# Performance work log

Hardware: AMD Instinct MI355X
Metric: run time of the kernel (lower is better)

The kernel has to match this reference:

```python
import jax, jax.numpy as jnp
import numpy as np

N, E, G = 50000, 800000, 64
F_IN, H = 128, 256


def setup_inputs() -> dict:
    key = jax.random.key(0)
    ks = jax.random.split(key, 16)
    s = 0.05
    return {
        "x": jax.random.normal(ks[0], (N, F_IN), jnp.float32),
        "edge_index": jax.random.randint(ks[1], (2, E), 0, N, jnp.int32),
        "batch": jnp.sort(jax.random.randint(ks[2], (N,), 0, G, jnp.int32)),
        "W1": jax.random.normal(ks[3], (F_IN, H), jnp.float32) * s,
        "b1": jnp.zeros((H,), jnp.float32),
        "W2": jax.random.normal(ks[4], (H, H), jnp.float32) * s,
        "b2": jnp.zeros((H,), jnp.float32),
        "W3": jax.random.normal(ks[5], (H, H), jnp.float32) * s,
        "b3": jnp.zeros((H,), jnp.float32),
        "Wc1": jax.random.normal(ks[6], (2 * H, 512), jnp.float32) * s,
        "bc1": jnp.zeros((512,), jnp.float32),
        "Wc2": jax.random.normal(ks[7], (512, 256), jnp.float32) * s,
        "bc2": jnp.zeros((256,), jnp.float32),
        "Wc3": jax.random.normal(ks[8], (256, 5), jnp.float32) * s,
        "bc3": jnp.zeros((5,), jnp.float32),
    }


def _gcn_conv(x, src, dst, dis, W, b):
    # PyG GCNConv: h = x W; out = D^{-1/2}(A+I)D^{-1/2} h + b
    h = x @ W                                        # [N, H]
    coef = (dis[src] * dis[dst])[:, None]            # [E, 1]
    agg = jax.ops.segment_sum(h[src] * coef, dst, num_segments=x.shape[0])
    return agg + h * (dis * dis)[:, None] + b        # self-loop term


def reference(x, edge_index, batch, W1, b1, W2, b2, W3, b3,
              Wc1, bc1, Wc2, bc2, Wc3, bc3):
    src, dst = edge_index[0], edge_index[1]
    # degree with self loops (in-degree at dst, as PyG)
    deg = jax.ops.segment_sum(jnp.ones_like(dst, jnp.float32), dst,
                              num_segments=x.shape[0]) + 1.0
    dis = jax.lax.rsqrt(deg)                         # D^{-1/2}

    h = jax.nn.relu(_gcn_conv(x, src, dst, dis, W1, b1))  # dropout=identity (eval)
    h = jax.nn.relu(_gcn_conv(h, src, dst, dis, W2, b2))
    h = jax.nn.relu(_gcn_conv(h, src, dst, dis, W3, b3))

    # global mean / max pool per graph
    cnt = jax.ops.segment_sum(jnp.ones_like(batch, jnp.float32), batch,
                              num_segments=G)
    x_mean = jax.ops.segment_sum(h, batch, num_segments=G) / jnp.maximum(cnt, 1.0)[:, None]
    x_max = jax.ops.segment_max(h, batch, num_segments=G)
    x_max = jnp.where(cnt[:, None] > 0, x_max, 0.0)  # guard empty segments
    g = jnp.concatenate([x_mean, x_max], axis=1)     # [G, 512]

    g = jax.nn.relu(g @ Wc1 + bc1)
    g = jax.nn.relu(g @ Wc2 + bc2)
    return g @ Wc3 + bc3                             # [G, 5]
```

## Files before the change

### kernel.cpp

```cpp
#include <hip/hip_runtime.h>
#include <cstdint>

#define CDIV(a, b) (((a) + (b) - 1) / (b))

typedef short bf16x8 __attribute__((ext_vector_type(8)));
typedef float f32x4 __attribute__((ext_vector_type(4)));

__device__ inline ushort f2bf_rn(float f) {
    uint32_t u = __float_as_uint(f);
    uint32_t rounding = 0x7FFF + ((u >> 16) & 1);
    return (ushort)((u + rounding) >> 16);
}
__device__ inline float bf2f(ushort h) { return __uint_as_float((uint32_t)h << 16); }

__global__ void k_init(int* __restrict__ degc, int N, float* __restrict__ sumbuf,
                       int* __restrict__ maxbuf, int PB) {
    int i = blockIdx.x * blockDim.x + threadIdx.x;
    if (i < N) degc[i] = 0;
    if (i < PB) { sumbuf[i] = 0.f; maxbuf[i] = 0; }
}

__global__ void k_deg(const int* __restrict__ dst, int E, int* __restrict__ degc) {
    int e = blockIdx.x * blockDim.x + threadIdx.x;
    if (e < E) atomicAdd(&degc[dst[e]], 1);
}

__global__ void k_xsplit(const float* __restrict__ x, int n, ushort* __restrict__ xhi) {
    int i = blockIdx.x * blockDim.x + threadIdx.x;
    if (i < n) xhi[i] = f2bf_rn(x[i]);
}

__global__ void k_scan_partial(const int* __restrict__ degc, int N, int* __restrict__ csum) {
    __shared__ int sm[256];
    int t = threadIdx.x;
    int idx = blockIdx.x * 1024 + t * 4;
    int s = 0;
#pragma unroll
    for (int j = 0; j < 4; ++j)
        if (idx + j < N) s += degc[idx + j];
    sm[t] = s;
    __syncthreads();
    for (int off = 128; off > 0; off >>= 1) {
        if (t < off) sm[t] += sm[t + off];
        __syncthreads();
    }
    if (t == 0) csum[blockIdx.x] = sm[0];
}

__global__ void k_scan_chunks(const int* __restrict__ csum, int nch, int* __restrict__ coff,
                              int* __restrict__ row_ptr, int N, int E) {
    if (threadIdx.x == 0 && blockIdx.x == 0) {
        int run = 0;
        for (int i = 0; i < nch; ++i) { coff[i] = run; run += csum[i]; }
        row_ptr[N] = E;
    }
}

__global__ void k_scan_final(const int* __restrict__ degc, int N, const int* __restrict__ coff,
                             int* __restrict__ row_ptr, int* __restrict__ fill,
                             float* __restrict__ dis) {
    __shared__ int sm[256];
    int t = threadIdx.x;
    int idx = blockIdx.x * 1024 + t * 4;
    int v[4];
    int s = 0;
#pragma unroll
    for (int j = 0; j < 4; ++j) {
        v[j] = (idx + j < N) ? degc[idx + j] : 0;
        s += v[j];
    }
    sm[t] = s;
    __syncthreads();
    for (int off = 1; off < 256; off <<= 1) {
        int x = (t >= off) ? sm[t - off] : 0;
        __syncthreads();
        sm[t] += x;
        __syncthreads();
    }
    int excl = sm[t] - s + coff[blockIdx.x];
#pragma unroll
    for (int j = 0; j < 4; ++j) {
        if (idx + j < N) {
            row_ptr[idx + j] = excl;
            fill[idx + j] = 0;
            dis[idx + j] = rsqrtf((float)v[j] + 1.0f);
            excl += v[j];
        }
    }
}

__global__ void k_fill(const int* __restrict__ src, const int* __restrict__ dst, int E,
                       const int* __restrict__ row_ptr, int* __restrict__ fill,
                       int* __restrict__ esrc) {
    int e = blockIdx.x * blockDim.x + threadIdx.x;
    if (e >= E) return;
    int d = dst[e], s = src[e];
    int pos = row_ptr[d] + atomicAdd(&fill[d], 1);
    esrc[pos] = s;
}

template <int C, bool SELF_F32>
__global__ __launch_bounds__(256) void k_agg(const float* __restrict__ xf,
                                             const ushort* __restrict__ hhi,
                                             const float* __restrict__ dis,
                                             const int* __restrict__ row_ptr,
                                             const int* __restrict__ esrc, int N,
                                             ushort* __restrict__ ohi,
                                             ushort* __restrict__ olo) {
    constexpr int V = C / 64;
    int wave = (blockIdx.x * blockDim.x + threadIdx.x) >> 6;
    int lane = threadIdx.x & 63;
    if (wave >= N) return;
    const int i = wave;
    const float di = dis[i];
    const float dd = di * di;
    float acc[V];
    if constexpr (SELF_F32) {
        const float* xr = xf + (size_t)i * C + lane * V;
        if constexpr (V == 4) {
            float4 v = *reinterpret_cast<const float4*>(xr);
            acc[0] = dd * v.x; acc[1] = dd * v.y; acc[2] = dd * v.z; acc[3] = dd * v.w;
        } else {
            float2 v = *reinterpret_cast<const float2*>(xr);
            acc[0] = dd * v.x; acc[1] = dd * v.y;
        }
    } else {
        size_t sb = (size_t)i * C + lane * V;
        if constexpr (V == 4) {
            ushort4 h = *reinterpret_cast<const ushort4*>(hhi + sb);
            acc[0] = dd * bf2f(h.x); acc[1] = dd * bf2f(h.y);
            acc[2] = dd * bf2f(h.z); acc[3] = dd * bf2f(h.w);
        } else {
            ushort2 h = *reinterpret_cast<const ushort2*>(hhi + sb);
            acc[0] = dd * bf2f(h.x); acc[1] = dd * bf2f(h.y);
        }
    }
    const int p0 = row_ptr[i], p1 = row_ptr[i + 1];
    int p = p0;
    if constexpr (V == 4) {
        for (; p + 4 <= p1; p += 4) {
            int s0 = esrc[p], s1 = esrc[p + 1], s2 = esrc[p + 2], s3 = esrc[p + 3];
            float c0 = dis[s0] * di, c1 = dis[s1] * di, c2 = dis[s2] * di, c3 = dis[s3] * di;
            ushort4 v0 = *reinterpret_cast<const ushort4*>(hhi + (size_t)s0 * C + lane * V);
            ushort4 v1 = *reinterpret_cast<const ushort4*>(hhi + (size_t)s1 * C + lane * V);
            ushort4 v2 = *reinterpret_cast<const ushort4*>(hhi + (size_t)s2 * C + lane * V);
            ushort4 v3 = *reinterpret_cast<const ushort4*>(hhi + (size_t)s3 * C + lane * V);
            acc[0] += c0 * bf2f(v0.x); acc[1] += c0 * bf2f(v0.y);
            acc[2] += c0 * bf2f(v0.z); acc[3] += c0 * bf2f(v0.w);
            acc[0] += c1 * bf2f(v1.x); acc[1] += c1 * bf2f(v1.y);
            acc[2] += c1 * bf2f(v1.z); acc[3] += c1 * bf2f(v1.w);
            acc[0] += c2 * bf2f(v2.x); acc[1] += c2 * bf2f(v2.y);
            acc[2] += c2 * bf2f(v2.z); acc[3] += c2 * bf2f(v2.w);
            acc[0] += c3 * bf2f(v3.x); acc[1] += c3 * bf2f(v3.y);
            acc[2] += c3 * bf2f(v3.z); acc[3] += c3 * bf2f(v3.w);
        }
        for (; p < p1; ++p) {
            int s = esrc[p];
            float c = dis[s] * di;
            ushort4 v = *reinterpret_cast<const ushort4*>(hhi + (size_t)s * C + lane * V);
            acc[0] += c * bf2f(v.x); acc[1] += c * bf2f(v.y);
            acc[2] += c * bf2f(v.z); acc[3] += c * bf2f(v.w);
        }
    } else {
        for (; p + 4 <= p1; p += 4) {
            int s0 = esrc[p], s1 = esrc[p + 1], s2 = esrc[p + 2], s3 = esrc[p + 3];
            float c0 = dis[s0] * di, c1 = dis[s1] * di, c2 = dis[s2] * di, c3 = dis[s3] * di;
            ushort2 v0 = *reinterpret_cast<const ushort2*>(hhi + (size_t)s0 * C + lane * V);
            ushort2 v1 = *reinterpret_cast<const ushort2*>(hhi + (size_t)s1 * C + lane * V);
            ushort2 v2 = *reinterpret_cast<const ushort2*>(hhi + (size_t)s2 * C + lane * V);
            ushort2 v3 = *reinterpret_cast<const ushort2*>(hhi + (size_t)s3 * C + lane * V);
            acc[0] += c0 * bf2f(v0.x); acc[1] += c0 * bf2f(v0.y);
            acc[0] += c1 * bf2f(v1.x); acc[1] += c1 * bf2f(v1.y);
            acc[0] += c2 * bf2f(v2.x); acc[1] += c2 * bf2f(v2.y);
            acc[0] += c3 * bf2f(v3.x); acc[1] += c3 * bf2f(v3.y);
        }
        for (; p < p1; ++p) {
            int s = esrc[p];
            float c = dis[s] * di;
            ushort2 v = *reinterpret_cast<const ushort2*>(hhi + (size_t)s * C + lane * V);
            acc[0] += c * bf2f(v.x); acc[1] += c * bf2f(v.y);
        }
    }
    ushort hi[V], lo[V];
#pragma unroll
    for (int j = 0; j < V; ++j) {
        hi[j] = f2bf_rn(acc[j]);
        lo[j] = f2bf_rn(acc[j] - bf2f(hi[j]));
    }
    size_t ob = (size_t)i * C + lane * V;
    if constexpr (V == 4) {
        *reinterpret_cast<ushort4*>(ohi + ob) = make_ushort4(hi[0], hi[1], hi[2], hi[3]);
        *reinterpret_cast<ushort4*>(olo + ob) = make_ushort4(lo[0], lo[1], lo[2], lo[3]);
    } else {
        *reinterpret_cast<ushort2*>(ohi + ob) = make_ushort2(hi[0], hi[1]);
        *reinterpret_cast<ushort2*>(olo + ob) = make_ushort2(lo[0], lo[1]);
    }
}

__global__ void k_wsplit(const float* __restrict__ W, int K, ushort* __restrict__ Whi,
                         ushort* __restrict__ Wlo) {
    int idx = blockIdx.x * 256 + threadIdx.x;
    if (idx >= K * 256) return;
    int k = idx >> 8, n = idx & 255;
    float v = W[idx];
    ushort hi = f2bf_rn(v);
    ushort lo = f2bf_rn(v - bf2f(hi));
    int ks = k >> 5, r = k & 31;
    int lane = (r >> 3) * 16 + (n & 15);
    int j = r & 7;
    size_t d = (((size_t)ks * 16 + (n >> 4)) * 64 + lane) * 8 + j;
    Whi[d] = hi;
    Wlo[d] = lo;
}

template <int K, bool POOL>
__global__ __launch_bounds__(256) void k_gemm_bf16(const ushort* __restrict__ Ahi,
                                                   const ushort* __restrict__ Alo,
                                                   const ushort* __restrict__ Whi,
                                                   const ushort* __restrict__ Wlo,
                                                   const float* __restrict__ bias, int M,
                                                   ushort* __restrict__ Hhi,
                                                   const int* __restrict__ batch,
                                                   float* __restrict__ sumbuf,
                                                   int* __restrict__ maxbuf) {
    __shared__ ushort Bs[2][2][8][512];
    const int t = threadIdx.x;
    const int w = t >> 6, lane = t & 63;
    constexpr int KS = K / 32;

    const int nwg = (int)gridDim.x;
    const int orig = (int)blockIdx.x;
    const int q = nwg >> 3, r = nwg & 7;
    const int xcd = orig & 7;
    const int swz = (xcd < r ? xcd * (q + 1) : r * (q + 1) + (xcd - r) * q) + (orig >> 3);
    const int bm = (swz >> 1) * 64;
    const int bn = (swz & 1) * 128;
    const int rw = bm + w * 16;

    f32x4 acc[8] = {};

    int row0 = min(rw + (lane & 15), M - 1);
    const int kbase = (lane >> 4) * 8;
    const ushort* pa0h = Ahi + (size_t)row0 * K + kbase;
    const ushort* pa0l = Alo + (size_t)row0 * K + kbase;
    const int nf0 = bn >> 4;

    bf16x8 sbh[2], sbl[2];
    auto loadB = [&](int ks) {
#pragma unroll
        for (int q2 = 0; q2 < 2; ++q2) {
            int nf = (w << 1) | q2;
            size_t widx = (((size_t)ks * 16 + nf0 + nf) * 64 + lane) * 8;
            sbh[q2] = *reinterpret_cast<const bf16x8*>(Whi + widx);
            sbl[q2] = *reinterpret_cast<const bf16x8*>(Wlo + widx);
        }
    };
    auto writeB = [&](int b) {
#pragma unroll
        for (int q2 = 0; q2 < 2; ++q2) {
            int nf = (w << 1) | q2;
            *reinterpret_cast<bf16x8*>(&Bs[b][0][nf][lane * 8]) = sbh[q2];
            *reinterpret_cast<bf16x8*>(&Bs[b][1][nf][lane * 8]) = sbl[q2];
        }
    };

    bf16x8 c0h, c0l, n0h, n0l, m0h, m0l;
    auto loadA = [&](int ks, bf16x8& xh, bf16x8& xl) {
        xh = *reinterpret_cast<const bf16x8*>(pa0h + ks * 32);
        xl = *reinterpret_cast<const bf16x8*>(pa0l + ks * 32);
    };

    loadB(0);
    writeB(0);
    loadA(0, c0h, c0l);
    if (KS > 1) loadA(1, n0h, n0l);
    if (KS > 1) loadB(1);
    __syncthreads();

#pragma unroll
    for (int ks = 0; ks < KS; ++ks) {
        const int buf = ks & 1;
        if (ks + 2 < KS) loadA(ks + 2, m0h, m0l);
#pragma unroll
        for (int nf = 0; nf < 8; ++nf) {
            bf16x8 bh = *reinterpret_cast<const bf16x8*>(&Bs[buf][0][nf][lane * 8]);
            bf16x8 bl = *reinterpret_cast<const bf16x8*>(&Bs[buf][1][nf][lane * 8]);
            acc[nf] = __builtin_amdgcn_mfma_f32_16x16x32_bf16(c0h, bh, acc[nf], 0, 0, 0);
            acc[nf] = __builtin_amdgcn_mfma_f32_16x16x32_bf16(c0h, bl, acc[nf], 0, 0, 0);
            acc[nf] = __builtin_amdgcn_mfma_f32_16x16x32_bf16(c0l, bh, acc[nf], 0, 0, 0);
        }
        if (ks + 1 < KS) {
            writeB(buf ^ 1);
            if (ks + 2 < KS) loadB(ks + 2);
            __syncthreads();
            c0h = n0h; c0l = n0l;
            n0h = m0h; n0l = m0l;
        }
    }

    const int colq = lane & 15;
    const int rowq = (lane >> 4) * 4;

    if constexpr (!POOL) {
#pragma unroll
        for (int nf = 0; nf < 8; ++nf) {
            int col = bn + nf * 16 + colq;
            float bia = bias[col];
#pragma unroll
            for (int r2 = 0; r2 < 4; ++r2) {
                int rr = rw + rowq + r2;
                if (rr < M) {
                    float v = fmaxf(acc[nf][r2] + bia, 0.f);
                    Hhi[(size_t)rr * 256 + col] = f2bf_rn(v);
                }
            }
        }
    } else {
        int r0 = min(rw + rowq, M - 1);
        int r3 = min(rw + rowq + 3, M - 1);
        int g0 = batch[r0];
        int g3 = batch[r3];
        int gfirst = __shfl(g0, 0);
        bool uni = __all(g0 == gfirst && g3 == gfirst);
        if (uni) {
#pragma unroll
            for (int nf = 0; nf < 8; ++nf) {
                int col = bn + nf * 16 + colq;
                float bia = bias[col];
                float s = 0.f, mx = 0.f;
#pragma unroll
                for (int r2 = 0; r2 < 4; ++r2) {
                    int rr = rw + rowq + r2;
                    float v = fmaxf(acc[nf][r2] + bia, 0.f);
                    if (rr < M) { s += v; mx = fmaxf(mx, v); }
                }
                s += __shfl_xor(s, 16);
                mx = fmaxf(mx, __shfl_xor(mx, 16));
                s += __shfl_xor(s, 32);
                mx = fmaxf(mx, __shfl_xor(mx, 32));
                if ((lane >> 4) == 0) {
                    atomicAdd(&sumbuf[gfirst * 256 + col], s);
                    atomicMax(&maxbuf[gfirst * 256 + col], __float_as_int(mx));
                }
            }
        } else {
#pragma unroll
            for (int nf = 0; nf < 8; ++nf) {
                int col = bn + nf * 16 + colq;
                float bia = bias[col];
#pragma unroll
                for (int r2 = 0; r2 < 4; ++r2) {
                    int rr = rw + rowq + r2;
                    if (rr < M) {
                        float v = fmaxf(acc[nf][r2] + bia, 0.f);
                        int g = batch[rr];
                        atomicAdd(&sumbuf[g * 256 + col], v);
                        atomicMax(&maxbuf[g * 256 + col], __float_as_int(v));
                    }
                }
            }
        }
    }
}

__global__ __launch_bounds__(512) void k_head(const float* __restrict__ sumbuf,
                                              const int* __restrict__ maxbuf,
                                              const int* __restrict__ batch, int N,
                                              const float* __restrict__ Wc1,
                                              const float* __restrict__ bc1,
                                              const float* __restrict__ Wc2,
                                              const float* __restrict__ bc2,
                                              const float* __restrict__ Wc3,
                                              const float* __restrict__ bc3,
                                              float* __restrict__ out) {
    __shared__ float gf[512];
    __shared__ float h1[512];
    __shared__ float h2[256];
    __shared__ int cntS;
    const int g = blockIdx.x;
    const int t = threadIdx.x;

    if (t == 0) {
        int lo = 0, hi = N;
        while (lo < hi) { int mid = (lo + hi) >> 1; if (batch[mid] < g) lo = mid + 1; else hi = mid; }
        int s = lo;
        lo = 0; hi = N;
        while (lo < hi) { int mid = (lo + hi) >> 1; if (batch[mid] < g + 1) lo = mid + 1; else hi = mid; }
        cntS = lo - s;
    }
    __syncthreads();
    const int cnt = cntS;
    if (t < 256) {
        float mean = sumbuf[g * 256 + t] / fmaxf((float)cnt, 1.0f);
        float mx = __int_as_float(maxbuf[g * 256 + t]);
        if (cnt == 0) { mean = 0.f; mx = 0.f; }
        gf[t] = mean;
        gf[256 + t] = mx;
    }
    __syncthreads();
    {
        float a0 = 0.f, a1 = 0.f, a2 = 0.f, a3 = 0.f;
        for (int k = 0; k < 512; k += 4) {
            a0 += gf[k + 0] * Wc1[(size_t)(k + 0) * 512 + t];
            a1 += gf[k + 1] * Wc1[(size_t)(k + 1) * 512 + t];
            a2 += gf[k + 2] * Wc1[(size_t)(k + 2) * 512 + t];
            a3 += gf[k + 3] * Wc1[(size_t)(k + 3) * 512 + t];
        }
        h1[t] = fmaxf((a0 + a1) + (a2 + a3) + bc1[t], 0.f);
    }
    __syncthreads();
    if (t < 256) {
        float a0 = 0.f, a1 = 0.f, a2 = 0.f, a3 = 0.f;
        for (int k = 0; k < 512; k += 4) {
            a0 += h1[k + 0] * Wc2[(size_t)(k + 0) * 256 + t];
            a1 += h1[k + 1] * Wc2[(size_t)(k + 1) * 256 + t];
            a2 += h1[k + 2] * Wc2[(size_t)(k + 2) * 256 + t];
            a3 += h1[k + 3] * Wc2[(size_t)(k + 3) * 256 + t];
        }
        h2[t] = fmaxf((a0 + a1) + (a2 + a3) + bc2[t], 0.f);
    }
    __syncthreads();
    if (t < 5) {
        float a = bc3[t];
        for (int k = 0; k < 256; ++k) a += h2[k] * Wc3[(size_t)k * 5 + t];
        out[(size_t)g * 5 + t] = a;
    }
}

extern "C" void kernel_launch(void* const* d_in, const int* in_sizes, int n_in, void* d_out,
                              int out_size, void* d_ws, size_t ws_size, hipStream_t stream) {
    const float* x = (const float*)d_in[0];
    const int* eidx = (const int*)d_in[1];
    const int* batch = (const int*)d_in[2];
    const float* W1 = (const float*)d_in[3];
    const float* b1 = (const float*)d_in[4];
    const float* W2 = (const float*)d_in[5];
    const float* b2 = (const float*)d_in[6];
    const float* W3 = (const float*)d_in[7];
    const float* b3 = (const float*)d_in[8];
    const float* Wc1 = (const float*)d_in[9];
    const float* bc1 = (const float*)d_in[10];
    const float* Wc2 = (const float*)d_in[11];
    const float* bc2 = (const float*)d_in[12];
    const float* Wc3 = (const float*)d_in[13];
    const float* bc3 = (const float*)d_in[14];
    float* out = (float*)d_out;

    const int N = in_sizes[2];
    const int E = in_sizes[1] / 2;
    const int G = out_size / 5;
    const int* src = eidx;
    const int* dst = eidx + E;

    char* p = (char*)d_ws;
    auto alloc = [&](size_t bytes) {
        void* r = (void*)p;
        p += (bytes + 255) & ~(size_t)255;
        return r;
    };
    float* dis = (float*)alloc((size_t)N * 4);
    int* degc = (int*)alloc((size_t)N * 4);
    int* row_ptr = (int*)alloc((size_t)(N + 1) * 4);
    int* fill = (int*)alloc((size_t)N * 4);
    const int nch = CDIV(N, 1024);
    int* csum = (int*)alloc((size_t)nch * 4);
    int* coff = (int*)alloc((size_t)nch * 4);
    int* esrc = (int*)alloc((size_t)E * 4);
    float* sumbuf = (float*)alloc((size_t)G * 256 * 4);
    int* maxbuf = (int*)alloc((size_t)G * 256 * 4);
    ushort* Ahi = (ushort*)alloc((size_t)N * 256 * 2);
    ushort* Alo = (ushort*)alloc((size_t)N * 256 * 2);
    ushort* Hhi = (ushort*)alloc((size_t)N * 256 * 2);
    ushort* Xhi = (ushort*)alloc((size_t)N * 128 * 2);
    ushort* W1hi = (ushort*)alloc((size_t)128 * 256 * 2);
    ushort* W1lo = (ushort*)alloc((size_t)128 * 256 * 2);
    ushort* W2hi = (ushort*)alloc((size_t)256 * 256 * 2);
    ushort* W2lo = (ushort*)alloc((size_t)256 * 256 * 2);
    ushort* W3hi = (ushort*)alloc((size_t)256 * 256 * 2);
    ushort* W3lo = (ushort*)alloc((size_t)256 * 256 * 2);
    (void)ws_size;

    k_init<<<CDIV(N, 256), 256, 0, stream>>>(degc, N, sumbuf, maxbuf, G * 256);

    k_wsplit<<<CDIV(128 * 256, 256), 256, 0, stream>>>(W1, 128, W1hi, W1lo);
    k_wsplit<<<CDIV(256 * 256, 256), 256, 0, stream>>>(W2, 256, W2hi, W2lo);
    k_wsplit<<<CDIV(256 * 256, 256), 256, 0, stream>>>(W3, 256, W3hi, W3lo);
    k_xsplit<<<CDIV(N * 128, 256), 256, 0, stream>>>(x, N * 128, Xhi);

    k_deg<<<CDIV(E, 256), 256, 0, stream>>>(dst, E, degc);
    k_scan_partial<<<nch, 256, 0, stream>>>(degc, N, csum);
    k_scan_chunks<<<1, 64, 0, stream>>>(csum, nch, coff, row_ptr, N, E);
    k_scan_final<<<nch, 256, 0, stream>>>(degc, N, coff, row_ptr, fill, dis);
    k_fill<<<CDIV(E, 256), 256, 0, stream>>>(src, dst, E, row_ptr, fill, esrc);

    const int ggrid = CDIV(N, 64) * 2;

    k_agg<128, true><<<CDIV(N * 64, 256), 256, 0, stream>>>(x, Xhi, dis, row_ptr, esrc, N,
                                                            Ahi, Alo);
    k_gemm_bf16<128, false><<<ggrid, 256, 0, stream>>>(Ahi, Alo, W1hi, W1lo, b1, N, Hhi,
                                                       batch, sumbuf, maxbuf);
    k_agg<256, false><<<CDIV(N * 64, 256), 256, 0, stream>>>(nullptr, Hhi, dis, row_ptr,
                                                             esrc, N, Ahi, Alo);
    k_gemm_bf16<256, false><<<ggrid, 256, 0, stream>>>(Ahi, Alo, W2hi, W2lo, b2, N, Hhi,
                                                       batch, sumbuf, maxbuf);
    k_agg<256, false><<<CDIV(N * 64, 256), 256, 0, stream>>>(nullptr, Hhi, dis, row_ptr,
                                                             esrc, N, Ahi, Alo);
    k_gemm_bf16<256, true><<<ggrid, 256, 0, stream>>>(Ahi, Alo, W3hi, W3lo, b3, N, Hhi,
                                                      batch, sumbuf, maxbuf);

    k_head<<<G, 512, 0, stream>>>(sumbuf, maxbuf, batch, N, Wc1, bc1, Wc2, bc2, Wc3, bc3, out);
}
```

Baseline: 418.6 us.

## Narrow GEMM tiles to 64 columns and split classifier head into two kernels

The GEMM block tile shrinks from 64x128 to 64x64. The grid gets four column tiles per row block, and each wave now stages one B fragment instead of two. This doubles the number of workgroups and halves accumulator registers, aiming at higher occupancy, but each A tile is loaded twice as often. The classifier head is also split into k_head1, which runs the first layer across 2*G blocks, and k_head2, which runs the remaining layers. This spreads the small head work over more blocks at the cost of an extra launch and an intermediate buffer.

```diff
diff --git a/kernel.cpp b/kernel.cpp
--- a/kernel.cpp
+++ b/kernel.cpp
@@ -223,7 +223,7 @@
                                                    const int* __restrict__ batch,
                                                    float* __restrict__ sumbuf,
                                                    int* __restrict__ maxbuf) {
-    __shared__ ushort Bs[2][2][8][512];
+    __shared__ ushort Bs[2][2][4][512];
     const int t = threadIdx.x;
     const int w = t >> 6, lane = t & 63;
     constexpr int KS = K / 32;
@@ -233,11 +233,11 @@
     const int q = nwg >> 3, r = nwg & 7;
     const int xcd = orig & 7;
     const int swz = (xcd < r ? xcd * (q + 1) : r * (q + 1) + (xcd - r) * q) + (orig >> 3);
-    const int bm = (swz >> 1) * 64;
-    const int bn = (swz & 1) * 128;
+    const int bm = (swz >> 2) * 64;
+    const int bn = (swz & 3) * 64;
     const int rw = bm + w * 16;
 
-    f32x4 acc[8] = {};
+    f32x4 acc[4] = {};
 
     int row0 = min(rw + (lane & 15), M - 1);
     const int kbase = (lane >> 4) * 8;
@@ -245,23 +245,15 @@
     const ushort* pa0l = Alo + (size_t)row0 * K + kbase;
     const int nf0 = bn >> 4;
 
-    bf16x8 sbh[2], sbl[2];
+    bf16x8 sbh, sbl;
     auto loadB = [&](int ks) {
-#pragma unroll
-        for (int q2 = 0; q2 < 2; ++q2) {
-            int nf = (w << 1) | q2;
-            size_t widx = (((size_t)ks * 16 + nf0 + nf) * 64 + lane) * 8;
-            sbh[q2] = *reinterpret_cast<const bf16x8*>(Whi + widx);
-            sbl[q2] = *reinterpret_cast<const bf16x8*>(Wlo + widx);
-        }
+        size_t widx = (((size_t)ks * 16 + nf0 + w) * 64 + lane) * 8;
+        sbh = *reinterpret_cast<const bf16x8*>(Whi + widx);
+        sbl = *reinterpret_cast<const bf16x8*>(Wlo + widx);
     };
     auto writeB = [&](int b) {
-#pragma unroll
-        for (int q2 = 0; q2 < 2; ++q2) {
-            int nf = (w << 1) | q2;
-            *reinterpret_cast<bf16x8*>(&Bs[b][0][nf][lane * 8]) = sbh[q2];
-            *reinterpret_cast<bf16x8*>(&Bs[b][1][nf][lane * 8]) = sbl[q2];
-        }
+        *reinterpret_cast<bf16x8*>(&Bs[b][0][w][lane * 8]) = sbh;
+        *reinterpret_cast<bf16x8*>(&Bs[b][1][w][lane * 8]) = sbl;
     };
 
     bf16x8 c0h, c0l, n0h, n0l, m0h, m0l;
@@ -282,7 +274,7 @@
         const int buf = ks & 1;
         if (ks + 2 < KS) loadA(ks + 2, m0h, m0l);
 #pragma unroll
-        for (int nf = 0; nf < 8; ++nf) {
+        for (int nf = 0; nf < 4; ++nf) {
             bf16x8 bh = *reinterpret_cast<const bf16x8*>(&Bs[buf][0][nf][lane * 8]);
             bf16x8 bl = *reinterpret_cast<const bf16x8*>(&Bs[buf][1][nf][lane * 8]);
             acc[nf] = __builtin_amdgcn_mfma_f32_16x16x32_bf16(c0h, bh, acc[nf], 0, 0, 0);
@@ -303,7 +295,7 @@
 
     if constexpr (!POOL) {
 #pragma unroll
-        for (int nf = 0; nf < 8; ++nf) {
+        for (int nf = 0; nf < 4; ++nf) {
             int col = bn + nf * 16 + colq;
             float bia = bias[col];
 #pragma unroll
@@ -324,7 +316,7 @@
         bool uni = __all(g0 == gfirst && g3 == gfirst);
         if (uni) {
 #pragma unroll
-            for (int nf = 0; nf < 8; ++nf) {
+            for (int nf = 0; nf < 4; ++nf) {
                 int col = bn + nf * 16 + colq;
                 float bia = bias[col];
                 float s = 0.f, mx = 0.f;
@@ -345,7 +337,7 @@
             }
         } else {
 #pragma unroll
-            for (int nf = 0; nf < 8; ++nf) {
+            for (int nf = 0; nf < 4; ++nf) {
                 int col = bn + nf * 16 + colq;
                 float bia = bias[col];
 #pragma unroll
@@ -363,21 +355,16 @@
     }
 }
 
-__global__ __launch_bounds__(512) void k_head(const float* __restrict__ sumbuf,
-                                              const int* __restrict__ maxbuf,
-                                              const int* __restrict__ batch, int N,
-                                              const float* __restrict__ Wc1,
-                                              const float* __restrict__ bc1,
-                                              const float* __restrict__ Wc2,
-                                              const float* __restrict__ bc2,
-                                              const float* __restrict__ Wc3,
-                                              const float* __restrict__ bc3,
-                                              float* __restrict__ out) {
+__global__ __launch_bounds__(256) void k_head1(const float* __restrict__ sumbuf,
+                                               const int* __restrict__ maxbuf,
+                                               const int* __restrict__ batch, int N,
+                                               const float* __restrict__ Wc1,
+                                               const float* __restrict__ bc1,
+                                               float* __restrict__ h1buf) {
     __shared__ float gf[512];
-    __shared__ float h1[512];
-    __shared__ float h2[256];
     __shared__ int cntS;
-    const int g = blockIdx.x;
+    const int g = blockIdx.x >> 1;
+    const int half = blockIdx.x & 1;
     const int t = threadIdx.x;
 
     if (t == 0) {
@@ -390,7 +377,7 @@
     }
     __syncthreads();
     const int cnt = cntS;
-    if (t < 256) {
+    {
         float mean = sumbuf[g * 256 + t] / fmaxf((float)cnt, 1.0f);
         float mx = __int_as_float(maxbuf[g * 256 + t]);
         if (cnt == 0) { mean = 0.f; mx = 0.f; }
@@ -398,18 +385,31 @@
         gf[256 + t] = mx;
     }
     __syncthreads();
+    const int o = half * 256 + t;
+    float a0 = 0.f, a1 = 0.f, a2 = 0.f, a3 = 0.f;
+    for (int k = 0; k < 512; k += 4) {
+        a0 += gf[k + 0] * Wc1[(size_t)(k + 0) * 512 + o];
+        a1 += gf[k + 1] * Wc1[(size_t)(k + 1) * 512 + o];
+        a2 += gf[k + 2] * Wc1[(size_t)(k + 2) * 512 + o];
+        a3 += gf[k + 3] * Wc1[(size_t)(k + 3) * 512 + o];
+    }
+    h1buf[(size_t)g * 512 + o] = fmaxf((a0 + a1) + (a2 + a3) + bc1[o], 0.f);
+}
+
+__global__ __launch_bounds__(256) void k_head2(const float* __restrict__ h1buf,
+                                               const float* __restrict__ Wc2,
+                                               const float* __restrict__ bc2,
+                                               const float* __restrict__ Wc3,
+                                               const float* __restrict__ bc3,
+                                               float* __restrict__ out) {
+    __shared__ float h1[512];
+    __shared__ float h2[256];
+    const int g = blockIdx.x;
+    const int t = threadIdx.x;
+    h1[t] = h1buf[(size_t)g * 512 + t];
+    h1[256 + t] = h1buf[(size_t)g * 512 + 256 + t];
+    __syncthreads();
     {
-        float a0 = 0.f, a1 = 0.f, a2 = 0.f, a3 = 0.f;
-        for (int k = 0; k < 512; k += 4) {
-            a0 += gf[k + 0] * Wc1[(size_t)(k + 0) * 512 + t];
-            a1 += gf[k + 1] * Wc1[(size_t)(k + 1) * 512 + t];
-            a2 += gf[k + 2] * Wc1[(size_t)(k + 2) * 512 + t];
-            a3 += gf[k + 3] * Wc1[(size_t)(k + 3) * 512 + t];
-        }
-        h1[t] = fmaxf((a0 + a1) + (a2 + a3) + bc1[t], 0.f);
-    }
-    __syncthreads();
-    if (t < 256) {
         float a0 = 0.f, a1 = 0.f, a2 = 0.f, a3 = 0.f;
         for (int k = 0; k < 512; k += 4) {
             a0 += h1[k + 0] * Wc2[(size_t)(k + 0) * 256 + t];
@@ -468,6 +468,7 @@
     int* esrc = (int*)alloc((size_t)E * 4);
     float* sumbuf = (float*)alloc((size_t)G * 256 * 4);
     int* maxbuf = (int*)alloc((size_t)G * 256 * 4);
+    float* h1buf = (float*)alloc((size_t)G * 512 * 4);
     ushort* Ahi = (ushort*)alloc((size_t)N * 256 * 2);
     ushort* Alo = (ushort*)alloc((size_t)N * 256 * 2);
     ushort* Hhi = (ushort*)alloc((size_t)N * 256 * 2);
@@ -493,7 +494,7 @@
     k_scan_final<<<nch, 256, 0, stream>>>(degc, N, coff, row_ptr, fill, dis);
     k_fill<<<CDIV(E, 256), 256, 0, stream>>>(src, dst, E, row_ptr, fill, esrc);
 
-    const int ggrid = CDIV(N, 64) * 2;
+    const int ggrid = CDIV(N, 64) * 4;
 
     k_agg<128, true><<<CDIV(N * 64, 256), 256, 0, stream>>>(x, Xhi, dis, row_ptr, esrc, N,
                                                             Ahi, Alo);
@@ -508,5 +509,6 @@
     k_gemm_bf16<256, true><<<ggrid, 256, 0, stream>>>(Ahi, Alo, W3hi, W3lo, b3, N, Hhi,
                                                       batch, sumbuf, maxbuf);
 
-    k_head<<<G, 512, 0, stream>>>(sumbuf, maxbuf, batch, N, Wc1, bc1, Wc2, bc2, Wc3, bc3, out);
-}
+    k_head1<<<G * 2, 256, 0, stream>>>(sumbuf, maxbuf, batch, N, Wc1, bc1, h1buf);
+    k_head2<<<G, 256, 0, stream>>>(h1buf, Wc2, bc2, Wc3, bc3, out);
+}
```

After: 425.8 us. No clear change (+1.7%).
